# Performance work log

Hardware: AMD Instinct MI355X
Metric: run time of the kernel (lower is better)

## Reference

```python
import jax, jax.numpy as jnp
import numpy as np
import math

B, N, DIM, H, DH = 4, 1024, 512, 8, 64
INNER = H * DH
TEMP = 0.1
REG_LAMBDA = 0.3
LARGE_NEG = -1.0e9


def setup_inputs() -> dict:
    key = jax.random.key(0)
    ks = jax.random.split(key, 10)
    x = jax.random.normal(ks[0], (B, N, DIM), dtype=jnp.float32)
    # binary channel mask with guaranteed self-connection on the diagonal
    m = jax.random.randint(ks[1], (B, N, N), 0, 2, dtype=jnp.int32)
    eye_i = jnp.eye(N, dtype=jnp.int32)[None]
    attn_mask = jnp.maximum(m, eye_i)
    s = 0.02
    Wq = jax.random.normal(ks[2], (DIM, INNER), dtype=jnp.float32) * s
    bq = jnp.zeros((INNER,), dtype=jnp.float32)
    Wk = jax.random.normal(ks[3], (DIM, INNER), dtype=jnp.float32) * s
    bk = jnp.zeros((INNER,), dtype=jnp.float32)
    Wv = jax.random.normal(ks[4], (DIM, INNER), dtype=jnp.float32) * s
    bv = jnp.zeros((INNER,), dtype=jnp.float32)
    Wo = jax.random.normal(ks[5], (INNER, DIM), dtype=jnpp_dummy()) * s if False else jax.random.normal(ks[5], (INNER, DIM), dtype=jnp.float32) * s
    bo = jnp.zeros((DIM,), dtype=jnp.float32)
    return {"x": x, "attn_mask": attn_mask, "Wq": Wq, "bq": bq, "Wk": Wk,
            "bk": bk, "Wv": Wv, "bv": bv, "Wo": Wo, "bo": bo}


def jnp_dummy():
    return jnp.float32


def _split_heads(t):
    # [b, n, h*d] -> [b, h, n, d]
    return t.reshape(t.shape[0], t.shape[1], H, DH).transpose(0, 2, 1, 3)


def _dynamical_contrastive_loss(scores, attn_mask_f, norm_matrix):
    # cosine similarity matrix (scores / |q||k|)
    cos = scores / norm_matrix
    e = jnp.exp(cos / TEMP)                                   # [b,h,n,n]
    pos = (e * attn_mask_f[:, None]).sum(-1)                  # [b,h,n]
    allsum = e.sum(-1)                                        # [b,h,n]
    clustering = -jnp.log(pos / allsum)
    eye = jnp.eye(N, dtype=attn_mask_f.dtype)
    regular = jnp.abs(attn_mask_f - eye[None]).sum((-2, -1)) / (N * (N - 1))
    return clustering.mean() + REG_LAMBDA * regular.mean()


def reference(x, attn_mask, Wq, bq, Wk, bk, Wv, bv, Wo, bo):
    q = _split_heads(x @ Wq + bq)  # [b,h,n,d]
    k = _split_heads(x @ Wk + bk)
    v = _split_heads(x @ Wv + bv)
    scale = 1.0 / math.sqrt(DH)

    scores = jnp.einsum('bhid,bhjd->bhij', q, k)
    q_norm = jnp.linalg.norm(q, axis=-1, keepdims=True)       # [b,h,n,1]
    k_norm = jnp.linalg.norm(k, axis=-1, keepdims=True)
    norm_matrix = q_norm * jnp.swapaxes(k_norm, -1, -2)       # [b,h,n,n]

    am = attn_mask.astype(scores.dtype)[:, None]              # [b,1,n,n]
    masked_scores = scores * am + (1.0 - am) * LARGE_NEG
    # faithful replication of the all-blocked-row special case
    # (-1e9 is finite so this is a no-op unless scores contain -inf)
    row_all_blocked = jnp.all(jnp.isneginf(masked_scores), axis=-1, keepdims=True)
    masked_scores = jnp.where(row_all_blocked, jnp.zeros_like(masked_scores), masked_scores)

    dcl = _dynamical_contrastive_loss(scores, attn_mask.astype(scores.dtype), norm_matrix)

    attn = jax.nn.softmax(masked_scores * scale, axis=-1)
    out = jnp.einsum('bhij,bhjd->bhid', attn, v)
    out = out.transpose(0, 2, 1, 3).reshape(x.shape[0], x.shape[1], INNER)
    # dropout is identity in eval mode
    return out @ Wo + bo, attn, dcl
```

## Files before the change

kernel.cpp:

```cpp
#include <hip/hip_runtime.h>
#include <hip/hip_bf16.h>
#include <math.h>

#define BB 4
#define NTOK 1024
#define DIMD 512
#define HH 8
#define DH 64
#define INNER 512
#define BH (BB*HH)
#define ROWS (BB*NTOK)
#define SCALE 0.125f
#define INV_TEMP 10.0f

typedef __bf16 bf16_t;
using bf16x4 = __attribute__((ext_vector_type(4))) __bf16;
using bf16x8 = __attribute__((ext_vector_type(8))) __bf16;
using f32x4  = __attribute__((ext_vector_type(4))) float;

__device__ __forceinline__ int swz(int row, int e) { return e ^ ((row & 7) << 3); }

__device__ __forceinline__ void gload_lds16(const bf16_t* g, bf16_t* l)
{
    __builtin_amdgcn_global_load_lds(
        (const __attribute__((address_space(1))) void*)g,
        (__attribute__((address_space(3))) void*)l, 16, 0, 0);
}

template<int TM, int TN, int MT, int NT>
__device__ __forceinline__ void gemm_core(
    const bf16_t* __restrict__ A, int ldA,
    const bf16_t* __restrict__ B, int ldB, int K,
    bf16_t* As, bf16_t* Bs, f32x4 (&acc)[MT][NT])
{
    const int t = threadIdx.x;
    const int w = t >> 6, l = t & 63;
    constexpr int WGN = TN / (NT * 16);
    const int wm = w / WGN, wn = w % WGN;
    const int lrow = l & 15, lk = (l >> 4) * 8;
    constexpr int ASZ = TM * 32, BSZ = TN * 32;

    auto stage = [&](int k0, int buf) {
        #pragma unroll
        for (int it = 0; it < TM / 64; ++it)
            gload_lds16(&A[(size_t)((t >> 2) + it * 64) * ldA + k0 + (t & 3) * 8],
                        As + buf * ASZ + ((size_t)it * 256 + w * 64) * 8);
        #pragma unroll
        for (int it = 0; it < TN / 64; ++it)
            gload_lds16(&B[(size_t)((t >> 2) + it * 64) * ldB + k0 + (t & 3) * 8],
                        Bs + buf * BSZ + ((size_t)it * 256 + w * 64) * 8);
    };

    stage(0, 0);
    __syncthreads();
    for (int k0 = 0; k0 < K; k0 += 32) {
        const int cur = (k0 >> 5) & 1;
        if (k0 + 32 < K) stage(k0 + 32, cur ^ 1);
        const bf16_t* Ac = As + cur * ASZ;
        const bf16_t* Bc = Bs + cur * BSZ;
        bf16x8 af[MT], bf[NT];
        #pragma unroll
        for (int mt = 0; mt < MT; ++mt)
            af[mt] = *(const bf16x8*)&Ac[(wm * MT * 16 + mt * 16 + lrow) * 32 + lk];
        #pragma unroll
        for (int nt = 0; nt < NT; ++nt)
            bf[nt] = *(const bf16x8*)&Bc[(wn * NT * 16 + nt * 16 + lrow) * 32 + lk];
        #pragma unroll
        for (int mt = 0; mt < MT; ++mt)
            #pragma unroll
            for (int nt = 0; nt < NT; ++nt)
                acc[mt][nt] = __builtin_amdgcn_mfma_f32_16x16x32_bf16(
                    af[mt], bf[nt], acc[mt][nt], 0, 0, 0);
        __syncthreads();
    }
}

__global__ __launch_bounds__(256) void prep_kernel(
    const float* __restrict__ x,
    const float* __restrict__ Wq, const float* __restrict__ Wk,
    const float* __restrict__ Wv, const float* __restrict__ Wo,
    const int* __restrict__ mask,
    bf16_t* __restrict__ xb, bf16_t* __restrict__ wt,
    unsigned int* __restrict__ mp)
{
    __shared__ float tile[32][33];
    const int bid = blockIdx.x, t = threadIdx.x;
    if (bid < 2048) {
        int idx = bid * 256 + t;
        float4 v = ((const float4*)x)[idx];
        bf16x4 o = { (bf16_t)v.x, (bf16_t)v.y, (bf16_t)v.z, (bf16_t)v.w };
        ((bf16x4*)xb)[idx] = o;
    } else if (bid < 3072) {
        int f = bid - 2048;
        int bx = f & 15, by = (f >> 4) & 15, z = f >> 8;
        const float* src = (z == 0) ? Wq : (z == 1) ? Wk : (z == 2) ? Wv : Wo;
        bf16_t* dst = wt + (size_t)z * DIMD * INNER;
        const int tx = t & 31, ty = t >> 5;
        const int rBase = by * 32, cBase = bx * 32;
        #pragma unroll
        for (int i = 0; i < 4; ++i)
            tile[ty + i * 8][tx] = src[(size_t)(rBase + ty + i * 8) * INNER + cBase + tx];
        __syncthreads();
        #pragma unroll
        for (int i = 0; i < 4; ++i)
            dst[(size_t)(cBase + ty + i * 8) * DIMD + rBase + tx] = (bf16_t)tile[tx][ty + i * 8];
    } else {
        int f = bid - 3072;
        int rr = f & 255, b = f >> 8;
        const int* mb = mask + ((size_t)(b * NTOK + rr * 4)) * NTOK;
        #pragma unroll
        for (int u = 0; u < 4; ++u) {
            int col = u * 256 + t;
            unsigned int o = (unsigned)mb[col]
                           | ((unsigned)mb[NTOK + col] << 8)
                           | ((unsigned)mb[2 * NTOK + col] << 16)
                           | ((unsigned)mb[3 * NTOK + col] << 24);
            mp[((size_t)b * 256 + rr) * NTOK + col] = o;
        }
    }
}

__global__ __launch_bounds__(256) void qkv_gemm(
    const bf16_t* __restrict__ xb, const bf16_t* __restrict__ wt,
    const float* __restrict__ bq, const float* __restrict__ bk,
    const float* __restrict__ bv,
    bf16_t* __restrict__ qb, bf16_t* __restrict__ kb, bf16_t* __restrict__ vt,
    float* __restrict__ iqn, float* __restrict__ ikn)
{
    __shared__ __align__(16) bf16_t As[2 * 64 * 32];
    __shared__ __align__(16) bf16_t Bs[2 * 128 * 32];
    const int z = blockIdx.z;
    const bf16_t* Bp = wt + (size_t)z * DIMD * INNER;
    const float* bias = (z == 0) ? bq : (z == 1) ? bk : bv;
    const int rowBase = blockIdx.y * 64, colBase = blockIdx.x * 128;

    f32x4 acc[2][4] = {};
    gemm_core<64, 128, 2, 4>(xb + (size_t)rowBase * DIMD, DIMD,
                             Bp + (size_t)colBase * DIMD, DIMD, DIMD,
                             As, Bs, acc);

    const int l = threadIdx.x & 63, w = threadIdx.x >> 6;
    const int wm = w >> 1, wn = w & 1;
    float nsum[2][4] = {};
    #pragma unroll
    for (int mt = 0; mt < 2; ++mt)
        #pragma unroll
        for (int nt = 0; nt < 4; ++nt)
            #pragma unroll
            for (int r = 0; r < 4; ++r) {
                int grow = rowBase + wm * 32 + mt * 16 + (l >> 4) * 4 + r;
                int gcol = colBase + wn * 64 + nt * 16 + (l & 15);
                float val = acc[mt][nt][r] + bias[gcol];
                bf16_t vb16 = (bf16_t)val;
                int b = grow >> 10, n = grow & 1023, h = gcol >> 6, d = gcol & 63;
                if (z == 0)
                    qb[(((size_t)b * HH + h) * NTOK + n) * DH + d] = vb16;
                else if (z == 1)
                    kb[(((size_t)b * HH + h) * NTOK + n) * DH + d] = vb16;
                else
                    vt[(((size_t)b * HH + h) * DH + d) * NTOK + n] = vb16;
                if (z < 2) { float vb = (float)vb16; nsum[mt][r] += vb * vb; }
            }
    if (z < 2) {
        float* dst = (z == 0) ? iqn : ikn;
        const int h = (colBase >> 6) + wn;
        #pragma unroll
        for (int mt = 0; mt < 2; ++mt)
            #pragma unroll
            for (int r = 0; r < 4; ++r) {
                float s = nsum[mt][r];
                s += __shfl_xor(s, 8); s += __shfl_xor(s, 4);
                s += __shfl_xor(s, 2); s += __shfl_xor(s, 1);
                if ((l & 15) == 0) {
                    int grow = rowBase + wm * 32 + mt * 16 + (l >> 4) * 4 + r;
                    int b = grow >> 10, n = grow & 1023;
                    dst[((size_t)b * HH + h) * NTOK + n] = 1.0f / sqrtf(s);
                }
            }
    }
}

__global__ __launch_bounds__(512, 6) void attn_fused(
    const bf16_t* __restrict__ qb, const bf16_t* __restrict__ kb,
    const bf16_t* __restrict__ vt, const unsigned int* __restrict__ mp,
    const float* __restrict__ iqn, const float* __restrict__ ikn,
    float* __restrict__ attnf, bf16_t* __restrict__ ctxb,
    float* __restrict__ cl, float* __restrict__ rg)
{
    __shared__ __align__(16) bf16_t Ks[2][64 * 64];
    __shared__ __align__(16) bf16_t Vs[2][64 * 64];
    __shared__ __align__(16) bf16_t Ps[8][16 * 64];
    __shared__ float4 sred[8][16];
    const int bh = blockIdx.y;
    const int b = bh >> 3, h = bh & 7;
    const int rowBase = blockIdx.x * 64;
    const bf16_t* Q = qb + (size_t)bh * NTOK * DH;
    const bf16_t* K = kb + (size_t)bh * NTOK * DH;
    const bf16_t* V = vt + (size_t)bh * DH * NTOK;
    const float* iknr = ikn + (size_t)bh * NTOK;
    const int t = threadIdx.x, w = t >> 6, l = t & 63;
    const int half = w >> 2, rw = w & 3;
    const int l15 = l & 15, q = l >> 4;
    bf16_t* Pw = Ps[w];

    bf16x8 af[2];
    {
        const bf16_t* qrow = Q + (size_t)(rowBase + rw * 16 + l15) * DH + q * 8;
        af[0] = *(const bf16x8*)(qrow);
        af[1] = *(const bf16x8*)(qrow + 32);
    }
    const int tok = rowBase + rw * 16 + q * 4;
    float iqn4[4];
    #pragma unroll
    for (int r = 0; r < 4; ++r)
        iqn4[r] = iqn[(size_t)bh * NTOK + tok + r];
    const unsigned int* mrow = mp + ((size_t)b * 256 + (tok >> 2)) * NTOK;

    float alls[4] = {}, pos[4] = {}, esum[4] = {}, regf[4] = {};

    for (int tt = 0; tt < 8; ++tt) {
        const int col0 = half * 512 + tt * 64;
        #pragma unroll
        for (int u = 0; u < 2; ++u) {
            int g = (u * 8 + w) * 64 + l;
            int hh = g >> 9, kr = (g >> 3) & 63, ci = g & 7;
            gload_lds16(K + (size_t)(hh * 512 + tt * 64 + kr) * DH + ((ci * 8) ^ ((kr & 7) << 3)),
                        &Ks[0][0] + (size_t)(u * 8 + w) * 512);
        }
        unsigned int mm4[4]; float ik4[4];
        #pragma unroll
        for (int nt = 0; nt < 4; ++nt) {
            int c = col0 + nt * 16 + l15;
            mm4[nt] = mrow[c];
            ik4[nt] = iknr[c];
        }
        __syncthreads();
        f32x4 sacc[4] = {};
        #pragma unroll
        for (int ks = 0; ks < 2; ++ks) {
            int koff = ks * 32 + q * 8;
            #pragma unroll
            for (int nt = 0; nt < 4; ++nt) {
                int kr = nt * 16 + l15;
                bf16x8 bfk = *(const bf16x8*)&Ks[half][kr * 64 + swz(kr, koff)];
                sacc[nt] = __builtin_amdgcn_mfma_f32_16x16x32_bf16(af[ks], bfk, sacc[nt], 0, 0, 0);
            }
        }
        #pragma unroll
        for (int nt = 0; nt < 4; ++nt) {
            float ik = ik4[nt];
            unsigned int mm = mm4[nt];
            #pragma unroll
            for (int r = 0; r < 4; ++r) {
                float s = sacc[nt][r];
                float mbit = (float)((mm >> (8 * r)) & 1u);
                float e1 = __expf(s * iqn4[r] * ik * INV_TEMP);
                float e2 = __expf(s * SCALE);
                alls[r] += e1;
                pos[r]  += e1 * mbit;
                esum[r] += e2 * mbit;
                regf[r] += mbit;
            }
        }
        __syncthreads();
    }
    #pragma unroll
    for (int r = 0; r < 4; ++r) {
        #pragma unroll
        for (int off = 8; off; off >>= 1) {
            alls[r] += __shfl_xor(alls[r], off);
            pos[r]  += __shfl_xor(pos[r], off);
            esum[r] += __shfl_xor(esum[r], off);
            regf[r] += __shfl_xor(regf[r], off);
        }
    }
    if (l15 == 0) {
        #pragma unroll
        for (int r = 0; r < 4; ++r)
            sred[w][q * 4 + r] = make_float4(alls[r], pos[r], esum[r], regf[r]);
    }
    __syncthreads();
    float inv4[4];
    #pragma unroll
    for (int r = 0; r < 4; ++r) {
        float4 o = sred[w ^ 4][q * 4 + r];
        float allsT = alls[r] + o.x;
        float posT  = pos[r]  + o.y;
        float esumT = esum[r] + o.z;
        float regT  = regf[r] + o.w;
        inv4[r] = 1.0f / esumT;
        if (half == 0 && l15 == 0) {
            int rowG = bh * NTOK + tok + r;
            cl[rowG] = logf(allsT) - logf(posT);
            if (h == 0) rg[b * NTOK + tok + r] = regT - 1.0f;
        }
    }

    float* prow = attnf + ((size_t)bh * NTOK + tok) * NTOK;
    f32x4 cacc[4] = {};
    for (int tt = 0; tt < 8; ++tt) {
        const int col0 = half * 512 + tt * 64;
        #pragma unroll
        for (int u = 0; u < 2; ++u) {
            int g = (u * 8 + w) * 64 + l;
            int hh = g >> 9, kr = (g >> 3) & 63, ci = g & 7;
            gload_lds16(K + (size_t)(hh * 512 + tt * 64 + kr) * DH + ((ci * 8) ^ ((kr & 7) << 3)),
                        &Ks[0][0] + (size_t)(u * 8 + w) * 512);
        }
        #pragma unroll
        for (int u = 0; u < 2; ++u) {
            int g = (u * 8 + w) * 64 + l;
            int hh = g >> 9, d = (g >> 3) & 63, ci = g & 7;
            gload_lds16(V + (size_t)d * NTOK + hh * 512 + tt * 64 + ((ci * 8) ^ ((d & 7) << 3)),
                        &Vs[0][0] + (size_t)(u * 8 + w) * 512);
        }
        unsigned int mm4[4];
        #pragma unroll
        for (int nt = 0; nt < 4; ++nt)
            mm4[nt] = mrow[col0 + nt * 16 + l15];
        __syncthreads();
        f32x4 sacc[4] = {};
        #pragma unroll
        for (int ks = 0; ks < 2; ++ks) {
            int koff = ks * 32 + q * 8;
            #pragma unroll
            for (int nt = 0; nt < 4; ++nt) {
                int kr = nt * 16 + l15;
                bf16x8 bfk = *(const bf16x8*)&Ks[half][kr * 64 + swz(kr, koff)];
                sacc[nt] = __builtin_amdgcn_mfma_f32_16x16x32_bf16(af[ks], bfk, sacc[nt], 0, 0, 0);
            }
        }
        #pragma unroll
        for (int nt = 0; nt < 4; ++nt) {
            int c = nt * 16 + l15;
            unsigned int mm = mm4[nt];
            #pragma unroll
            for (int r = 0; r < 4; ++r) {
                float p = ((mm >> (8 * r)) & 1u)
                        ? __expf(sacc[nt][r] * SCALE) * inv4[r] : 0.0f;
                prow[(size_t)r * NTOK + col0 + c] = p;
                int pr = q * 4 + r;
                Pw[pr * 64 + swz(pr, c)] = (bf16_t)p;
            }
        }
        #pragma unroll
        for (int ks = 0; ks < 2; ++ks) {
            int koff = ks * 32 + q * 8;
            bf16x8 afp = *(const bf16x8*)&Pw[l15 * 64 + swz(l15, koff)];
            #pragma unroll
            for (int nt = 0; nt < 4; ++nt) {
                int d = nt * 16 + l15;
                bf16x8 bfv = *(const bf16x8*)&Vs[half][d * 64 + swz(d, koff)];
                cacc[nt] = __builtin_amdgcn_mfma_f32_16x16x32_bf16(afp, bfv, cacc[nt], 0, 0, 0);
            }
        }
        __syncthreads();
    }
    float* cred = (float*)&Ps[0][0];
    if (half == 1) {
        #pragma unroll
        for (int nt = 0; nt < 4; ++nt)
            #pragma unroll
            for (int r = 0; r < 4; ++r)
                cred[(size_t)rw * 1024 + (q * 4 + r) * 64 + nt * 16 + l15] = cacc[nt][r];
    }
    __syncthreads();
    if (half == 0) {
        #pragma unroll
        for (int nt = 0; nt < 4; ++nt)
            #pragma unroll
            for (int r = 0; r < 4; ++r) {
                float v = cacc[nt][r] + cred[(size_t)rw * 1024 + (q * 4 + r) * 64 + nt * 16 + l15];
                int n = tok + r;
                int d = nt * 16 + l15;
                ctxb[((size_t)b * NTOK + n) * INNER + h * DH + d] = (bf16_t)v;
            }
    }
}

__device__ __forceinline__ float block_sum(float v, float* sh)
{
    #pragma unroll
    for (int off = 32; off; off >>= 1) v += __shfl_down(v, off);
    __syncthreads();
    if ((threadIdx.x & 63) == 0) sh[threadIdx.x >> 6] = v;
    __syncthreads();
    return sh[0] + sh[1] + sh[2] + sh[3];
}

__global__ __launch_bounds__(256) void out_gemm(
    const bf16_t* __restrict__ ctxb, const bf16_t* __restrict__ wt,
    const float* __restrict__ bo, float* __restrict__ outp,
    const float* __restrict__ cl, const float* __restrict__ rg,
    float* __restrict__ dcl)
{
    __shared__ __align__(16) bf16_t As[2 * 64 * 32];
    __shared__ __align__(16) bf16_t Bs[2 * 128 * 32];
    __shared__ float sh4[4];
    const int rowBase = blockIdx.y * 64, colBase = blockIdx.x * 128;
    const bf16_t* Wot = wt + (size_t)3 * DIMD * INNER;

    f32x4 acc[2][4] = {};
    gemm_core<64, 128, 2, 4>(ctxb + (size_t)rowBase * INNER, INNER,
                             Wot + (size_t)colBase * INNER, INNER, INNER,
                             As, Bs, acc);

    const int l = threadIdx.x & 63, w = threadIdx.x >> 6;
    const int wm = w >> 1, wn = w & 1;
    #pragma unroll
    for (int mt = 0; mt < 2; ++mt)
        #pragma unroll
        for (int nt = 0; nt < 4; ++nt)
            #pragma unroll
            for (int r = 0; r < 4; ++r) {
                int grow = rowBase + wm * 32 + mt * 16 + (l >> 4) * 4 + r;
                int gcol = colBase + wn * 64 + nt * 16 + (l & 15);
                outp[(size_t)grow * DIMD + gcol] = acc[mt][nt][r] + bo[gcol];
            }

    if (blockIdx.x == 0 && blockIdx.y == 0) {
        float s1 = 0.f, s2 = 0.f;
        for (int idx = threadIdx.x; idx < BH * NTOK; idx += 256) s1 += cl[idx];
        for (int idx = threadIdx.x; idx < BB * NTOK; idx += 256) s2 += rg[idx];
        __syncthreads();
        s1 = block_sum(s1, sh4);
        s2 = block_sum(s2, sh4);
        if (threadIdx.x == 0) {
            dcl[0] = s1 * (1.0f / (float)(BB * HH * NTOK))
                   + 0.3f * s2 * (1.0f / ((float)NTOK * (float)(NTOK - 1) * (float)BB));
        }
    }
}

extern "C" void kernel_launch(void* const* d_in, const int* in_sizes, int n_in,
                              void* d_out, int out_size, void* d_ws, size_t ws_size,
                              hipStream_t stream)
{
    const float* x  = (const float*)d_in[0];
    const int* mask = (const int*)d_in[1];
    const float* Wq = (const float*)d_in[2];
    const float* bq = (const float*)d_in[3];
    const float* Wk = (const float*)d_in[4];
    const float* bk = (const float*)d_in[5];
    const float* Wv = (const float*)d_in[6];
    const float* bv = (const float*)d_in[7];
    const float* Wo = (const float*)d_in[8];
    const float* bo = (const float*)d_in[9];

    float* out   = (float*)d_out;
    float* attnf = out + (size_t)ROWS * DIMD;
    float* dcl   = attnf + (size_t)BH * NTOK * NTOK;

    char* wsb = (char*)d_ws;
    bf16_t* xb    = (bf16_t*)wsb;
    bf16_t* wt    = xb + (size_t)ROWS * DIMD;
    bf16_t* qb    = wt + (size_t)4 * DIMD * INNER;
    bf16_t* kb    = qb + (size_t)BH * NTOK * DH;
    bf16_t* vt    = kb + (size_t)BH * NTOK * DH;
    bf16_t* ctxb  = vt + (size_t)BH * NTOK * DH;
    float*  iqn   = (float*)(ctxb + (size_t)ROWS * INNER);
    float*  ikn   = iqn + BH * NTOK;
    float*  cl    = ikn + BH * NTOK;
    float*  rg    = cl + BH * NTOK;
    unsigned int* mpk = (unsigned int*)(rg + BB * NTOK);

    dim3 blk(256);
    prep_kernel<<<dim3(4096), blk, 0, stream>>>(x, Wq, Wk, Wv, Wo, mask, xb, wt, mpk);
    qkv_gemm<<<dim3(4, 64, 3), blk, 0, stream>>>(xb, wt, bq, bk, bv, qb, kb, vt, iqn, ikn);
    attn_fused<<<dim3(16, 32), dim3(512), 0, stream>>>(qb, kb, vt, mpk, iqn, ikn, attnf, ctxb, cl, rg);
    out_gemm<<<dim3(4, 64), blk, 0, stream>>>(ctxb, wt, bo, out, cl, rg, dcl);
}
```

Before: 309.7 us.

## Split fused attention into stats and PV kernels with vectorized attn stores

Splits the fused attention kernel into two launches. The first computes the row statistics (softmax denominator, contrastive loss terms, regularizer) and writes the inverse row sum to a workspace buffer. The second recomputes QK^T, stages fp32 probabilities through a padded LDS buffer so the large attention-matrix write can use coalesced 16-byte stores, and does the P·V MFMAs. This trades an extra launch and a re-read of the mask and K for lower LDS use per kernel and better global store coalescing on the dominant output write.

```diff
diff --git a/kernel.cpp b/kernel.cpp
--- a/kernel.cpp
+++ b/kernel.cpp
@@ -180,36 +180,31 @@
     }
 }
 
-__global__ __launch_bounds__(512, 6) void attn_fused(
+__global__ __launch_bounds__(512) void attn_stats(
     const bf16_t* __restrict__ qb, const bf16_t* __restrict__ kb,
-    const bf16_t* __restrict__ vt, const unsigned int* __restrict__ mp,
+    const unsigned int* __restrict__ mp,
     const float* __restrict__ iqn, const float* __restrict__ ikn,
-    float* __restrict__ attnf, bf16_t* __restrict__ ctxb,
-    float* __restrict__ cl, float* __restrict__ rg)
+    float* __restrict__ invE, float* __restrict__ cl, float* __restrict__ rg)
 {
     __shared__ __align__(16) bf16_t Ks[2][64 * 64];
-    __shared__ __align__(16) bf16_t Vs[2][64 * 64];
-    __shared__ __align__(16) bf16_t Ps[8][16 * 64];
     __shared__ float4 sred[8][16];
     const int bh = blockIdx.y;
     const int b = bh >> 3, h = bh & 7;
     const int rowBase = blockIdx.x * 64;
     const bf16_t* Q = qb + (size_t)bh * NTOK * DH;
     const bf16_t* K = kb + (size_t)bh * NTOK * DH;
-    const bf16_t* V = vt + (size_t)bh * DH * NTOK;
     const float* iknr = ikn + (size_t)bh * NTOK;
     const int t = threadIdx.x, w = t >> 6, l = t & 63;
-    const int half = w >> 2, rw = w & 3;
+    const int half = w >> 2;
     const int l15 = l & 15, q = l >> 4;
-    bf16_t* Pw = Ps[w];
 
     bf16x8 af[2];
     {
-        const bf16_t* qrow = Q + (size_t)(rowBase + rw * 16 + l15) * DH + q * 8;
+        const bf16_t* qrow = Q + (size_t)(rowBase + (w & 3) * 16 + l15) * DH + q * 8;
         af[0] = *(const bf16x8*)(qrow);
         af[1] = *(const bf16x8*)(qrow + 32);
     }
-    const int tok = rowBase + rw * 16 + q * 4;
+    const int tok = rowBase + (w & 3) * 16 + q * 4;
     float iqn4[4];
     #pragma unroll
     for (int r = 0; r < 4; ++r)
@@ -280,23 +275,55 @@
             sred[w][q * 4 + r] = make_float4(alls[r], pos[r], esum[r], regf[r]);
     }
     __syncthreads();
+    if (half == 0 && l15 == 0) {
+        #pragma unroll
+        for (int r = 0; r < 4; ++r) {
+            float4 o = sred[w ^ 4][q * 4 + r];
+            float allsT = alls[r] + o.x;
+            float posT  = pos[r]  + o.y;
+            float esumT = esum[r] + o.z;
+            float regT  = regf[r] + o.w;
+            int rowG = bh * NTOK + tok + r;
+            invE[rowG] = 1.0f / esumT;
+            cl[rowG] = logf(allsT) - logf(posT);
+            if (h == 0) rg[b * NTOK + tok + r] = regT - 1.0f;
+        }
+    }
+}
+
+__global__ __launch_bounds__(512) void attn_pav(
+    const bf16_t* __restrict__ qb, const bf16_t* __restrict__ kb,
+    const bf16_t* __restrict__ vt, const unsigned int* __restrict__ mp,
+    const float* __restrict__ invE,
+    float* __restrict__ attnf, bf16_t* __restrict__ ctxb)
+{
+    __shared__ __align__(16) bf16_t Ks[2][64 * 64];
+    __shared__ __align__(16) bf16_t Vs[2][64 * 64];
+    __shared__ __align__(16) float  Bn[8][16 * 36];
+    const int bh = blockIdx.y;
+    const int b = bh >> 3, h = bh & 7;
+    const int rowBase = blockIdx.x * 64;
+    const bf16_t* Q = qb + (size_t)bh * NTOK * DH;
+    const bf16_t* K = kb + (size_t)bh * NTOK * DH;
+    const bf16_t* V = vt + (size_t)bh * DH * NTOK;
+    const int t = threadIdx.x, w = t >> 6, l = t & 63;
+    const int half = w >> 2, rw = w & 3;
+    const int l15 = l & 15, q = l >> 4;
+    float* Bw = Bn[w];
+
+    bf16x8 af[2];
+    {
+        const bf16_t* qrow = Q + (size_t)(rowBase + rw * 16 + l15) * DH + q * 8;
+        af[0] = *(const bf16x8*)(qrow);
+        af[1] = *(const bf16x8*)(qrow + 32);
+    }
+    const int tok = rowBase + rw * 16 + q * 4;
     float inv4[4];
     #pragma unroll
-    for (int r = 0; r < 4; ++r) {
-        float4 o = sred[w ^ 4][q * 4 + r];
-        float allsT = alls[r] + o.x;
-        float posT  = pos[r]  + o.y;
-        float esumT = esum[r] + o.z;
-        float regT  = regf[r] + o.w;
-        inv4[r] = 1.0f / esumT;
-        if (half == 0 && l15 == 0) {
-            int rowG = bh * NTOK + tok + r;
-            cl[rowG] = logf(allsT) - logf(posT);
-            if (h == 0) rg[b * NTOK + tok + r] = regT - 1.0f;
-        }
-    }
-
-    float* prow = attnf + ((size_t)bh * NTOK + tok) * NTOK;
+    for (int r = 0; r < 4; ++r)
+        inv4[r] = invE[(size_t)bh * NTOK + tok + r];
+    const unsigned int* mrow = mp + ((size_t)b * 256 + (tok >> 2)) * NTOK;
+
     f32x4 cacc[4] = {};
     for (int tt = 0; tt < 8; ++tt) {
         const int col0 = half * 512 + tt * 64;
@@ -331,32 +358,42 @@
             }
         }
         #pragma unroll
-        for (int nt = 0; nt < 4; ++nt) {
-            int c = nt * 16 + l15;
-            unsigned int mm = mm4[nt];
-            #pragma unroll
-            for (int r = 0; r < 4; ++r) {
-                float p = ((mm >> (8 * r)) & 1u)
-                        ? __expf(sacc[nt][r] * SCALE) * inv4[r] : 0.0f;
-                prow[(size_t)r * NTOK + col0 + c] = p;
-                int pr = q * 4 + r;
-                Pw[pr * 64 + swz(pr, c)] = (bf16_t)p;
-            }
-        }
-        #pragma unroll
-        for (int ks = 0; ks < 2; ++ks) {
-            int koff = ks * 32 + q * 8;
-            bf16x8 afp = *(const bf16x8*)&Pw[l15 * 64 + swz(l15, koff)];
-            #pragma unroll
-            for (int nt = 0; nt < 4; ++nt) {
-                int d = nt * 16 + l15;
-                bf16x8 bfv = *(const bf16x8*)&Vs[half][d * 64 + swz(d, koff)];
-                cacc[nt] = __builtin_amdgcn_mfma_f32_16x16x32_bf16(afp, bfv, cacc[nt], 0, 0, 0);
-            }
-        }
-        __syncthreads();
-    }
-    float* cred = (float*)&Ps[0][0];
+        for (int hf = 0; hf < 2; ++hf) {
+            #pragma unroll
+            for (int ntl = 0; ntl < 2; ++ntl) {
+                int nt = hf * 2 + ntl;
+                unsigned int mm = mm4[nt];
+                #pragma unroll
+                for (int r = 0; r < 4; ++r) {
+                    float p = ((mm >> (8 * r)) & 1u)
+                            ? __expf(sacc[nt][r] * SCALE) * inv4[r] : 0.0f;
+                    Bw[(q * 4 + r) * 36 + ntl * 16 + l15] = p;
+                }
+            }
+            #pragma unroll
+            for (int i = 0; i < 2; ++i) {
+                int row = i * 8 + (l >> 3);
+                f32x4 v = *(const f32x4*)&Bw[row * 36 + 4 * (l & 7)];
+                *(f32x4*)&attnf[((size_t)bh * NTOK + rowBase + rw * 16 + row) * NTOK
+                                + col0 + hf * 32 + 4 * (l & 7)] = v;
+            }
+            {
+                f32x4 pa = *(const f32x4*)&Bw[l15 * 36 + q * 8];
+                f32x4 pb = *(const f32x4*)&Bw[l15 * 36 + q * 8 + 4];
+                bf16x8 afp = { (bf16_t)pa[0], (bf16_t)pa[1], (bf16_t)pa[2], (bf16_t)pa[3],
+                               (bf16_t)pb[0], (bf16_t)pb[1], (bf16_t)pb[2], (bf16_t)pb[3] };
+                int koff = hf * 32 + q * 8;
+                #pragma unroll
+                for (int nt = 0; nt < 4; ++nt) {
+                    int d = nt * 16 + l15;
+                    bf16x8 bfv = *(const bf16x8*)&Vs[half][d * 64 + swz(d, koff)];
+                    cacc[nt] = __builtin_amdgcn_mfma_f32_16x16x32_bf16(afp, bfv, cacc[nt], 0, 0, 0);
+                }
+            }
+        }
+        __syncthreads();
+    }
+    float* cred = (float*)&Ks[0][0];
     if (half == 1) {
         #pragma unroll
         for (int nt = 0; nt < 4; ++nt)
@@ -462,11 +499,13 @@
     float*  ikn   = iqn + BH * NTOK;
     float*  cl    = ikn + BH * NTOK;
     float*  rg    = cl + BH * NTOK;
-    unsigned int* mpk = (unsigned int*)(rg + BB * NTOK);
+    float*  invE  = rg + BB * NTOK;
+    unsigned int* mpk = (unsigned int*)(invE + BH * NTOK);
 
     dim3 blk(256);
     prep_kernel<<<dim3(4096), blk, 0, stream>>>(x, Wq, Wk, Wv, Wo, mask, xb, wt, mpk);
     qkv_gemm<<<dim3(4, 64, 3), blk, 0, stream>>>(xb, wt, bq, bk, bv, qb, kb, vt, iqn, ikn);
-    attn_fused<<<dim3(16, 32), dim3(512), 0, stream>>>(qb, kb, vt, mpk, iqn, ikn, attnf, ctxb, cl, rg);
+    attn_stats<<<dim3(16, 32), dim3(512), 0, stream>>>(qb, kb, mpk, iqn, ikn, invE, cl, rg);
+    attn_pav<<<dim3(16, 32), dim3(512), 0, stream>>>(qb, kb, vt, mpk, invE, attnf, ctxb);
     out_gemm<<<dim3(4, 64), blk, 0, stream>>>(ctxb, wt, bo, out, cl, rg, dcl);
 }
```

Result: faster. 278.9 us (-10.0%).
